# Kernel tuning notes

Measured on AMD Instinct MI355X. Metric: run time of the kernel, lower is better.

Reference implementation:

```python
import jax, jax.numpy as jnp
import numpy as np

DIM = 4096
N_HEADS = 32
N_KV_HEADS = 8
HEAD_DIM = DIM // N_HEADS  # 128
N_REP = N_HEADS // N_KV_HEADS  # 4
HIDDEN = 14336  # 4*dim -> 2/3 -> *1.3 -> round up to multiple of 256
EPS = 1e-6
BSZ, SEQLEN, CACHE_LEN = 1, 2048, 4096
ROPE_THETA = 500000.0


def setup_inputs() -> dict:
    key = jax.random.key(0)
    ks = jax.random.split(key, 16)
    s = 0.02
    x = jax.random.normal(ks[0], (BSZ, SEQLEN, DIM), jnp.float32)
    cache_k = jax.random.normal(ks[1], (BSZ, CACHE_LEN, N_KV_HEADS, HEAD_DIM), jnp.float32)
    cache_v = jax.random.normal(ks[2], (BSZ, CACHE_LEN, N_KV_HEADS, HEAD_DIM), jnp.float32)
    # causal mask over rolling cache: query i may attend to cache slot j <= (CACHE_LEN - SEQLEN) + i
    qi = jnp.arange(SEQLEN)[:, None]
    kj = jnp.arange(CACHE_LEN)[None, :]
    mask = jnp.where(kj <= (CACHE_LEN - SEQLEN) + qi, 0.0, -1e9).astype(jnp.float32)[None, None]
    # rotary freqs (cos/sin pairs) for the new seqlen positions (start of window here)
    inv = 1.0 / (ROPE_THETA ** (jnp.arange(0, HEAD_DIM, 2, dtype=jnp.float32) / HEAD_DIM))
    t = jnp.arange(SEQLEN, dtype=jnp.float32)
    ang = t[:, None] * inv[None, :]  # [S, HEAD_DIM//2]
    freqs_cis = jnp.stack([jnp.cos(ang), jnp.sin(ang)], axis=-1)  # [S, HD//2, 2]
    # params (stored as (in, out))
    wq = jax.random.normal(ks[3], (DIM, N_HEADS * HEAD_DIM), jnp.float32) * s
    wk = jax.random.normal(ks[4], (DIM, N_KV_HEADS * HEAD_DIM), jnp.float32) * s
    wv = jax.random.normal(ks[5], (DIM, N_KV_HEADS * HEAD_DIM), jnp.float32) * s
    wo = jax.random.normal(ks[6], (N_HEADS * HEAD_DIM, DIM), jnp.float32) * s
    w1 = jax.random.normal(ks[7], (DIM, HIDDEN), jnp.float32) * s
    w2 = jax.random.normal(ks[8], (HIDDEN, DIM), jnp.float32) * s
    w3 = jax.random.normal(ks[9], (DIM, HIDDEN), jnp.float32) * s
    attn_norm_w = jnp.ones((DIM,), jnp.float32)
    ffn_norm_w = jnp.ones((DIM,), jnp.float32)
    return dict(x=x, mask=mask, freqs_cis=freqs_cis, cache_k=cache_k, cache_v=cache_v,
                wq=wq, wk=wk, wv=wv, wo=wo, w1=w1, w2=w2, w3=w3,
                attn_norm_w=attn_norm_w, ffn_norm_w=ffn_norm_w)


def rmsnorm(x, w, eps=EPS):
    return x * jax.lax.rsqrt(jnp.mean(x * x, axis=-1, keepdims=True) + eps) * w


def apply_rope(xq, xk, freqs_cis):
    # xq: [B,S,Hq,D], xk: [B,S,Hkv,D]; freqs_cis: [S, D//2, 2]
    cos = freqs_cis[None, :, None, :, 0]  # [1,S,1,D//2]
    sin = freqs_cis[None, :, None, :, 1]
    def rot(t):
        tp = t.reshape(*t.shape[:-1], -1, 2)
        t0, t1 = tp[..., 0], tp[..., 1]
        o0 = t0 * cos - t1 * sin
        o1 = t0 * sin + t1 * cos
        return jnp.stack([o0, o1], axis=-1).reshape(t.shape)
    return rot(xq), rot(xk)


def reference(x, mask, freqs_cis, cache_k, cache_v, wq, wk, wv, wo, w1, w2, w3, attn_norm_w, ffn_norm_w):
    bsz, seqlen, _ = x.shape
    # --- attention norm ---
    xn = rmsnorm(x, attn_norm_w)
    # --- qkv ---
    xq = (xn @ wq).reshape(bsz, seqlen, N_HEADS, HEAD_DIM)
    xk = (xn @ wk).reshape(bsz, seqlen, N_KV_HEADS, HEAD_DIM)
    xv = (xn @ wv).reshape(bsz, seqlen, N_KV_HEADS, HEAD_DIM)
    xq, xk = apply_rope(xq, xk, freqs_cis)
    # --- rolling KV cache ---
    cache_k = jnp.concatenate([cache_k[:, seqlen:], xk], axis=1)  # [B,CL,Hkv,D]
    cache_v = jnp.concatenate([cache_v[:, seqlen:], xv], axis=1)
    keys = jnp.repeat(cache_k[:bsz], N_REP, axis=2)    # [B,CL,Hq,D]
    values = jnp.repeat(cache_v[:bsz], N_REP, axis=2)
    # --- attention ---
    scores = jnp.einsum('bqhd,bkhd->bhqk', xq, keys) / jnp.sqrt(jnp.float32(HEAD_DIM))
    scores = jax.nn.softmax(scores + mask, axis=-1)
    attn = jnp.einsum('bhqk,bkhd->bqhd', scores, values).reshape(bsz, seqlen, -1)
    h = x + attn @ wo
    # --- ffn (SwiGLU) ---
    hn = rmsnorm(h, ffn_norm_w)
    out = h + (jax.nn.silu(hn @ w1) * (hn @ w3)) @ w2
    return (out, cache_k, cache_v)
```

## Files before the change

kernel.cpp:

```cpp
#include <hip/hip_runtime.h>

typedef _Float16 h16;
typedef _Float16 h16x4 __attribute__((ext_vector_type(4)));
typedef _Float16 h16x8 __attribute__((ext_vector_type(8)));
typedef __fp16 fp16x2 __attribute__((ext_vector_type(2)));
typedef float f32x4 __attribute__((ext_vector_type(4)));
typedef float f32x16 __attribute__((ext_vector_type(16)));
typedef unsigned short u16;
typedef unsigned int u32;
typedef unsigned int u32x4 __attribute__((ext_vector_type(4)));

__device__ __forceinline__ f32x4 mfma16(h16x8 a, h16x8 b, f32x4 c) {
  return __builtin_amdgcn_mfma_f32_16x16x32_f16(a, b, c, 0, 0, 0);
}
__device__ __forceinline__ f32x16 mfma32(h16x8 a, h16x8 b, f32x16 c) {
  return __builtin_amdgcn_mfma_f32_32x32x16_f16(a, b, c, 0, 0, 0);
}
__device__ __forceinline__ float fexp2(float x) {
#if __has_builtin(__builtin_amdgcn_exp2f)
  return __builtin_amdgcn_exp2f(x);
#else
  return exp2f(x);
#endif
}
__device__ __forceinline__ u32 pkh(float a, float b) {
  fp16x2 t = __builtin_amdgcn_cvt_pkrtz(a, b);
  return __builtin_bit_cast(u32, t);
}

typedef const __attribute__((address_space(1))) void* gas_p;
typedef __attribute__((address_space(3))) void* las_p;
__device__ __forceinline__ void ldscp16(const void* g, void* l) {
  __builtin_amdgcn_global_load_lds((gas_p)g, (las_p)l, 16, 0, 0);
}
#define VMCNT(n) asm volatile("s_waitcnt vmcnt(" #n ")" ::: "memory")
#define SBAR() asm volatile("s_barrier" ::: "memory")

__global__ __launch_bounds__(256) void rmsnorm_k(
    const float* __restrict__ x, const float* __restrict__ w, h16* __restrict__ out) {
  const int row = blockIdx.x, t = threadIdx.x;
  const float* xr = x + (size_t)row * 4096;
  float4 v[4];
  float ss = 0.f;
#pragma unroll
  for (int j = 0; j < 4; j++) {
    v[j] = *(const float4*)(xr + 4 * t + 1024 * j);
    ss += v[j].x * v[j].x + v[j].y * v[j].y + v[j].z * v[j].z + v[j].w * v[j].w;
  }
#pragma unroll
  for (int off = 1; off < 64; off <<= 1) ss += __shfl_xor(ss, off, 64);
  __shared__ float red[4];
  if ((t & 63) == 0) red[t >> 6] = ss;
  __syncthreads();
  float scale = rsqrtf((red[0] + red[1] + red[2] + red[3]) * (1.f / 4096.f) + 1e-6f);
  h16* orow = out + (size_t)row * 4096;
#pragma unroll
  for (int j = 0; j < 4; j++) {
    float4 wv = *(const float4*)(w + 4 * t + 1024 * j);
    h16x4 o;
    o[0] = (h16)(v[j].x * scale * wv.x);
    o[1] = (h16)(v[j].y * scale * wv.y);
    o[2] = (h16)(v[j].z * scale * wv.z);
    o[3] = (h16)(v[j].w * scale * wv.w);
    *(h16x4*)(orow + 4 * t + 1024 * j) = o;
  }
}

__global__ __launch_bounds__(256) void convw_k(
    const float* __restrict__ W, h16* __restrict__ out, int rowN, int ktiles) {
  __shared__ u16 timg[8192];
  const int t = threadIdx.x, b = blockIdx.x, kt = blockIdx.y;
  const float* src = W + (size_t)(kt * 64) * rowN + b * 128;
#pragma unroll
  for (int i = 0; i < 8; i++) {
    int c = t + (i << 8);
    int krow = c >> 5, nc = (c & 31) << 2;
    float4 v = *(const float4*)(src + (size_t)krow * rowN + nc);
    int kc = krow >> 3, e = krow & 7;
    float vals[4] = {v.x, v.y, v.z, v.w};
#pragma unroll
    for (int j = 0; j < 4; j++) {
      int m = nc + j;
      h16 hv = (h16)vals[j];
      timg[(m << 6) + ((kc ^ (m & 7)) << 3) + e] = __builtin_bit_cast(u16, hv);
    }
  }
  __syncthreads();
  uint4* dst = (uint4*)(out + ((size_t)(b * ktiles + kt) << 13));
  const uint4* s4 = (const uint4*)timg;
#pragma unroll
  for (int i = 0; i < 4; i++) dst[t + (i << 8)] = s4[t + (i << 8)];
}

template <int EPI>
__global__ __launch_bounds__(512, 2) void gemm_k(
    const h16* __restrict__ A, const h16* __restrict__ Wt,
    float* outF, h16* outH, const float* resid, const h16* uin,
    int K, int lda, int ldo, int no0) {
  __shared__ u16 lds[3][24576];
  const int tid = threadIdx.x, lane = tid & 63;
  const int wv = tid >> 6, wr = wv >> 2, wc = wv & 3;
  const int g = lane >> 4, lr = lane & 15;
  const int m0 = blockIdx.y << 7, n0 = blockIdx.x << 8;
  const int ktiles = K >> 6;

  f32x4 acc[4][4];
#pragma unroll
  for (int i = 0; i < 4; i++)
#pragma unroll
    for (int j = 0; j < 4; j++) acc[i][j] = {0.f, 0.f, 0.f, 0.f};

  const int rA = tid >> 3;
  const int kcA = (tid & 7) ^ (rA & 7);
  const h16* gA = A + (size_t)(m0 + rA) * lda + (kcA << 3);
  const h16* gA2 = gA + (size_t)64 * lda;
  const h16* gB0 = Wt + (((size_t)(2 * blockIdx.x) * ktiles) << 13) + tid * 8;
  const h16* gB1 = Wt + (((size_t)(2 * blockIdx.x + 1) * ktiles) << 13) + tid * 8;

  auto issueA = [&](int t) {
    char* base = (char*)lds[t % 3];
    ldscp16(gA + t * 64, base + tid * 16);
    ldscp16(gA2 + t * 64, base + tid * 16 + 8192);
    ldscp16(gB0 + ((size_t)t << 13), base + 16384 + tid * 16);
    ldscp16(gB0 + ((size_t)t << 13) + 4096, base + 16384 + tid * 16 + 8192);
  };
  auto issueB = [&](int t) {
    char* base = (char*)lds[t % 3];
    ldscp16(gB1 + ((size_t)t << 13), base + 32768 + tid * 16);
    ldscp16(gB1 + ((size_t)t << 13) + 4096, base + 32768 + tid * 16 + 8192);
  };

  issueA(0); issueB(0); issueA(1); issueB(1);
  VMCNT(6);
  SBAR();

  for (int t = 0; t < ktiles; ++t) {
    const char* bp = (const char*)lds[t % 3];
    const bool more = (t + 2 < ktiles);
#pragma unroll
    for (int ks = 0; ks < 2; ++ks) {
      h16x8 av[4], bv[4];
      const int cc = (ks << 2) + g;
#pragma unroll
      for (int f = 0; f < 4; f++) {
        int row = (wr << 6) + (f << 4) + lr;
        av[f] = *(const h16x8*)(bp + row * 128 + ((cc ^ (row & 7)) << 4));
        int nr = (wc << 6) + (f << 4) + lr;
        bv[f] = *(const h16x8*)(bp + 16384 + nr * 128 + ((cc ^ (nr & 7)) << 4));
      }
      if (more) {
        if (ks == 0) issueA(t + 2);
        else issueB(t + 2);
      }
      __builtin_amdgcn_s_setprio(1);
#pragma unroll
      for (int fi = 0; fi < 4; fi++)
#pragma unroll
        for (int fj = 0; fj < 4; fj++)
          acc[fi][fj] = mfma16(av[fi], bv[fj], acc[fi][fj]);
      __builtin_amdgcn_s_setprio(0);
    }
    if (t + 1 < ktiles) {
      if (more) VMCNT(6);
      else VMCNT(0);
      SBAR();
    }
  }
#pragma unroll
  for (int fi = 0; fi < 4; fi++) {
    const int row = m0 + (wr << 6) + (fi << 4) + (g << 2);
#pragma unroll
    for (int fj = 0; fj < 4; fj++) {
      const int col = no0 + n0 + (wc << 6) + (fj << 4) + lr;
#pragma unroll
      for (int r = 0; r < 4; r++) {
        float vl = acc[fi][fj][r];
        if constexpr (EPI == 5) {
          if (col < 4096) outH[(size_t)(row + r) * 4096 + col] = (h16)vl;
          else outF[(size_t)(row + r) * 2048 + (col - 4096)] = vl;
        } else {
          size_t idx = (size_t)(row + r) * ldo + col;
          if constexpr (EPI == 1) outH[idx] = (h16)vl;
          else if constexpr (EPI == 2) outF[idx] = resid[idx] + vl;
          else if constexpr (EPI == 3) {
            float u = (float)uin[idx];
            outH[idx] = (h16)((u / (1.f + __expf(-u))) * vl);
          } else outF[idx] = outF[idx] + vl;
        }
      }
    }
  }
}

__global__ __launch_bounds__(256) void rope_q_k(
    const h16* __restrict__ qin, const float* __restrict__ freqs, h16* qout) {
  const int row = blockIdx.x, t = threadIdx.x;
  const float SCL = 0.12751743647239037f;
#pragma unroll
  for (int it = 0; it < 8; ++it) {
    int pid = t + 256 * it;
    int head = pid >> 6, pp = pid & 63;
    size_t idx = (size_t)row * 4096 + head * 128 + 2 * pp;
    float x0 = (float)qin[idx], x1 = (float)qin[idx + 1];
    float cs = freqs[row * 128 + 2 * pp], sn = freqs[row * 128 + 2 * pp + 1];
    qout[idx] = (h16)((x0 * cs - x1 * sn) * SCL);
    qout[idx + 1] = (h16)((x0 * sn + x1 * cs) * SCL);
  }
}

__global__ __launch_bounds__(256) void cache_build_k(
    const float* __restrict__ oldK, const float* __restrict__ oldV,
    const float* __restrict__ kvraw, const float* __restrict__ freqs,
    float* __restrict__ outK, float* __restrict__ outV,
    h16* __restrict__ Kf, h16* __restrict__ Vt) {
  const int rt = blockIdx.x, kvh = blockIdx.y;
  const int r0 = rt * 64, tid = threadIdx.x;
  __shared__ u16 vtile[64][128];
#pragma unroll
  for (int it = 0; it < 16; ++it) {
    int s = tid + 256 * it;
    int rr = s >> 6, pp = s & 63;
    int r = r0 + rr;
    float k0, k1, v0, v1;
    if (r < 2048) {
      const float* kp = oldK + (size_t)(r + 2048) * 1024 + kvh * 128 + 2 * pp;
      k0 = kp[0]; k1 = kp[1];
      const float* vp = oldV + (size_t)(r + 2048) * 1024 + kvh * 128 + 2 * pp;
      v0 = vp[0]; v1 = vp[1];
    } else {
      int tpos = r - 2048;
      const float* kp = kvraw + (size_t)tpos * 2048 + kvh * 128 + 2 * pp;
      float x0 = kp[0], x1 = kp[1];
      float cs = freqs[tpos * 128 + 2 * pp], sn = freqs[tpos * 128 + 2 * pp + 1];
      k0 = x0 * cs - x1 * sn;
      k1 = x0 * sn + x1 * cs;
      const float* vp = kvraw + (size_t)tpos * 2048 + 1024 + kvh * 128 + 2 * pp;
      v0 = vp[0]; v1 = vp[1];
    }
    size_t oidx = (size_t)r * 1024 + kvh * 128 + 2 * pp;
    outK[oidx] = k0; outK[oidx + 1] = k1;
    outV[oidx] = v0; outV[oidx + 1] = v1;
    size_t kfi = (size_t)kvh * 524288 + (size_t)r * 128 + 2 * pp;
    Kf[kfi] = (h16)k0; Kf[kfi + 1] = (h16)k1;
    h16 h0 = (h16)v0, h1 = (h16)v1;
    vtile[rr][2 * pp] = __builtin_bit_cast(u16, h0);
    vtile[rr][2 * pp + 1] = __builtin_bit_cast(u16, h1);
  }
  __syncthreads();
#pragma unroll
  for (int it = 0; it < 4; ++it) {
    int c = tid + 256 * it;
    int d = c >> 3, rg = c & 7;
    u16 tmp[8];
#pragma unroll
    for (int u = 0; u < 8; u++) tmp[u] = vtile[rg * 8 + u][d];
    *(uint4*)((u16*)Vt + (size_t)kvh * 524288 + (size_t)d * 4096 + r0 + rg * 8) =
        *(uint4*)tmp;
  }
}

__global__ __launch_bounds__(256, 2) void attn_k(
    const h16* __restrict__ Q, const h16* __restrict__ Kf,
    const h16* __restrict__ Vt, h16* __restrict__ O) {
  __shared__ u16 skv[2][16384];
  const int qt = 15 - blockIdx.x, h = blockIdx.y;
  const int q0 = qt << 7, kvh = h >> 2;
  const int tid = threadIdx.x, w = tid >> 6, lane = tid & 63;
  const int lq = lane & 31, lh = lane >> 5;
  const h16* Kb = Kf + (size_t)kvh * 524288;
  const h16* Vb = Vt + (size_t)kvh * 524288;
  const int qg = q0 + w * 32 + lq;

  h16x8 qv[8];
  {
    const h16* qp = Q + (size_t)qg * 4096 + h * 128 + (lh << 3);
#pragma unroll
    for (int c = 0; c < 8; c++) qv[c] = *(const h16x8*)(qp + c * 16);
  }
  h16x8 hone;
#pragma unroll
  for (int i = 0; i < 8; i++) hone[i] = (h16)1.0f;
  f32x16 oa[4], ol2;
#pragma unroll
  for (int d = 0; d < 4; d++)
#pragma unroll
    for (int v = 0; v < 16; v++) oa[d][v] = 0.f;
#pragma unroll
  for (int v = 0; v < 16; v++) ol2[v] = 0.f;
  float m2 = -3e38f;
  const int ntiles = 34 + 2 * qt;

  const int jK = tid >> 4, kch = tid & 15;
  const h16* gK = Kb + (size_t)jK * 128 + ((kch ^ (jK & 15)) << 3);
  const int dV = tid >> 3, jch = tid & 7;
  const h16* gV = Vb + (size_t)dV * 4096 + ((jch ^ (dV & 7)) << 3);

  auto issueK = [&](int jt) {
    char* base = (char*)skv[jt & 1];
    const h16* s = gK + (size_t)(jt << 6) * 128;
#pragma unroll
    for (int i = 0; i < 4; i++)
      ldscp16(s + (size_t)i * 2048, base + tid * 16 + i * 4096);
  };
  auto issueV = [&](int jt) {
    char* base = (char*)skv[jt & 1] + 16384;
    const h16* s = gV + (jt << 6);
#pragma unroll
    for (int i = 0; i < 4; i++)
      ldscp16(s + (size_t)i * 131072, base + tid * 16 + i * 4096);
  };

  issueK(0); issueV(0);
  VMCNT(0);
  SBAR();

  for (int jt = 0; jt < ntiles; ++jt) {
    const char* bp = (const char*)skv[jt & 1];
    const bool more = (jt + 1 < ntiles);
    if (more) issueK(jt + 1);
    f32x16 st[2];
#pragma unroll
    for (int jb = 0; jb < 2; jb++) {
      f32x16 s;
#pragma unroll
      for (int v = 0; v < 16; v++) s[v] = 0.f;
      const int jr = jb * 32 + lq;
      __builtin_amdgcn_s_setprio(1);
#pragma unroll
      for (int kc = 0; kc < 8; kc++) {
        h16x8 ak =
            *(const h16x8*)(bp + jr * 256 + ((((kc << 1) + lh) ^ (jr & 15)) << 4));
        s = mfma32(ak, qv[kc], s);
      }
      __builtin_amdgcn_s_setprio(0);
      st[jb] = s;
    }
    if (more) issueV(jt + 1);
    if (jt >= ntiles - 2) {
      const int j0 = jt << 6;
#pragma unroll
      for (int jb = 0; jb < 2; jb++)
#pragma unroll
        for (int v = 0; v < 16; v++) {
          int j = j0 + jb * 32 + (v & 3) + (((v >> 2) & 3) << 3) + (lh << 2);
          if (j > 2048 + qg) st[jb][v] = -1e30f;
        }
    }
    float pm = fmaxf(st[0][0], st[0][1]);
#pragma unroll
    for (int v = 2; v < 16; v += 2) pm = fmaxf(fmaxf(st[0][v], st[0][v + 1]), pm);
#pragma unroll
    for (int v = 0; v < 16; v += 2) pm = fmaxf(fmaxf(st[1][v], st[1][v + 1]), pm);
    pm = fmaxf(pm, __shfl_xor(pm, 32, 64));
    if (__any(pm - m2 > 8.f)) {
      float mn = fmaxf(m2, pm);
      float al = fexp2(m2 - mn);
      m2 = mn;
#pragma unroll
      for (int d = 0; d < 4; d++) oa[d] *= al;
      ol2 *= al;
    }
    u32 pw[2][8];
#pragma unroll
    for (int jb = 0; jb < 2; jb++)
#pragma unroll
      for (int c = 0; c < 4; c++) {
        float p0 = fexp2(st[jb][4 * c] - m2);
        float p1 = fexp2(st[jb][4 * c + 1] - m2);
        float p2 = fexp2(st[jb][4 * c + 2] - m2);
        float p3 = fexp2(st[jb][4 * c + 3] - m2);
        pw[jb][2 * c] = pkh(p0, p1);
        pw[jb][2 * c + 1] = pkh(p2, p3);
      }
    h16x8 pb[4];
#pragma unroll
    for (int kc = 0; kc < 4; kc++) {
      const int jb = kc >> 1, cb = (kc & 1) << 1;
      u32 oa_ = pw[jb][2 * cb], ob_ = pw[jb][2 * cb + 1];
      u32 oc_ = pw[jb][2 * cb + 2], od_ = pw[jb][2 * cb + 3];
      u32 s0 = lh ? oa_ : oc_, s1 = lh ? ob_ : od_;
      u32 r0 = __shfl_xor(s0, 32, 64), r1 = __shfl_xor(s1, 32, 64);
      u32x4 wds = {lh ? r0 : oa_, lh ? r1 : ob_, lh ? oc_ : r0, lh ? od_ : r1};
      pb[kc] = __builtin_bit_cast(h16x8, wds);
    }
    __builtin_amdgcn_s_setprio(1);
#pragma unroll
    for (int d = 0; d < 4; d++) {
      const int dr = (d << 5) + lq;
#pragma unroll
      for (int kc = 0; kc < 4; kc++) {
        h16x8 av = *(const h16x8*)(bp + 16384 + dr * 128 +
                                   ((((kc << 1) + lh) ^ (dr & 7)) << 4));
        oa[d] = mfma32(av, pb[kc], oa[d]);
      }
    }
#pragma unroll
    for (int kc = 0; kc < 4; kc++) ol2 = mfma32(hone, pb[kc], ol2);
    __builtin_amdgcn_s_setprio(0);
    if (more) {
      VMCNT(0);
      SBAR();
    }
  }
  float rl = 1.f / ol2[0];
  h16* Op = O + (size_t)qg * 4096 + h * 128;
#pragma unroll
  for (int d = 0; d < 4; d++)
#pragma unroll
    for (int b = 0; b < 4; b++) {
      h16x4 ov;
#pragma unroll
      for (int i = 0; i < 4; i++) ov[i] = (h16)(oa[d][(b << 2) + i] * rl);
      *(h16x4*)(Op + (d << 5) + (b << 3) + (lh << 2)) = ov;
    }
}

extern "C" void kernel_launch(void* const* d_in, const int* in_sizes, int n_in,
                              void* d_out, int out_size, void* d_ws, size_t ws_size,
                              hipStream_t stream) {
  const float* x = (const float*)d_in[0];
  const float* freqs = (const float*)d_in[2];
  const float* oldK = (const float*)d_in[3];
  const float* oldV = (const float*)d_in[4];
  const float* wq = (const float*)d_in[5];
  const float* wk = (const float*)d_in[6];
  const float* wvp = (const float*)d_in[7];
  const float* wo = (const float*)d_in[8];
  const float* w1 = (const float*)d_in[9];
  const float* w2 = (const float*)d_in[10];
  const float* w3 = (const float*)d_in[11];
  const float* anw = (const float*)d_in[12];
  const float* fnw = (const float*)d_in[13];
  float* out = (float*)d_out;
  float* outK = out + 8388608;
  float* outV = out + 12582912;

  char* ws = (char*)d_ws;
  h16* xn = (h16*)(ws + 0);
  h16* bufW = (h16*)(ws + 16777216);
  float* hbuf = (float*)(ws + 75497472);
  float* kvraw = (float*)(ws + 75497472);
  h16* kf = (h16*)(ws + 92274688);
  h16* vt = (h16*)(ws + 100663296);
  h16* ub = (h16*)(ws + 109051904);
  h16* qraw = (h16*)(ws + 109051904);
  h16* attnb = (h16*)(ws + 125829120);

  rmsnorm_k<<<2048, 256, 0, stream>>>(x, anw, xn);
  convw_k<<<dim3(32, 64), 256, 0, stream>>>(wq, bufW, 4096, 64);
  convw_k<<<dim3(8, 64), 256, 0, stream>>>(wk, bufW + ((size_t)32 * 64 << 13), 1024, 64);
  convw_k<<<dim3(8, 64), 256, 0, stream>>>(wvp, bufW + ((size_t)40 * 64 << 13), 1024, 64);
  gemm_k<5><<<dim3(24, 16), 512, 0, stream>>>(xn, bufW, kvraw, qraw, nullptr,
                                              nullptr, 4096, 4096, 0, 0);
  rope_q_k<<<2048, 256, 0, stream>>>(qraw, freqs, qraw);
  cache_build_k<<<dim3(64, 8), 256, 0, stream>>>(oldK, oldV, kvraw, freqs, outK,
                                                 outV, kf, vt);
  attn_k<<<dim3(16, 32), 256, 0, stream>>>(qraw, kf, vt, attnb);
  convw_k<<<dim3(32, 64), 256, 0, stream>>>(wo, bufW, 4096, 64);
  gemm_k<2><<<dim3(16, 16), 512, 0, stream>>>(attnb, bufW, hbuf, nullptr, x,
                                              nullptr, 4096, 4096, 4096, 0);
  rmsnorm_k<<<2048, 256, 0, stream>>>(hbuf, fnw, xn);
  convw_k<<<dim3(56, 64), 256, 0, stream>>>(w1, bufW, 14336, 64);
  gemm_k<1><<<dim3(28, 16), 512, 0, stream>>>(xn, bufW, nullptr, ub, nullptr,
                                              nullptr, 4096, 4096, 14336, 0);
  convw_k<<<dim3(56, 64), 256, 0, stream>>>(w1 + 7168, bufW, 14336, 64);
  gemm_k<1><<<dim3(28, 16), 512, 0, stream>>>(xn, bufW, nullptr, ub, nullptr,
                                              nullptr, 4096, 4096, 14336, 7168);
  convw_k<<<dim3(56, 64), 256, 0, stream>>>(w3, bufW, 14336, 64);
  gemm_k<3><<<dim3(28, 16), 512, 0, stream>>>(xn, bufW, nullptr, ub, nullptr, ub,
                                              4096, 4096, 14336, 0);
  convw_k<<<dim3(56, 64), 256, 0, stream>>>(w3 + 7168, bufW, 14336, 64);
  gemm_k<3><<<dim3(28, 16), 512, 0, stream>>>(xn, bufW, nullptr, ub, nullptr, ub,
                                              4096, 4096, 14336, 7168);
  convw_k<<<dim3(32, 112), 256, 0, stream>>>(w2, bufW, 4096, 112);
  gemm_k<2><<<dim3(16, 16), 512, 0, stream>>>(ub, bufW, out, nullptr, hbuf,
                                              nullptr, 7168, 14336, 4096, 0);
  convw_k<<<dim3(32, 112), 256, 0, stream>>>(w2 + (size_t)7168 * 4096, bufW, 4096, 112);
  gemm_k<4><<<dim3(16, 16), 512, 0, stream>>>(ub + 7168, bufW, out, nullptr,
                                              nullptr, nullptr, 7168, 14336, 4096, 0);
}
```

Baseline: 1.533 ms.

## Enlarge GEMM block tile to 256x256 with quadrant-staged double-buffered pipeline

The GEMM kernel changes from a 128x256 block tile with a 3-stage LDS ring to a 256x256 tile with a 2-stage double buffer. Each K-step is split into four quadrant MFMA phases, and loads for the next tile's A and B quadrants are interleaved between phases. The goal is to double operand reuse per block and cut global/L2 traffic per FLOP. In exchange each wave holds twice the accumulators (128 regs), which puts register pressure on the 2-blocks-per-CU bound. The grid is also halved, which may hurt wave balance across CUs for the smaller GEMMs.

Measured after the change: 1.718 ms. +12.1%, slower.

```diff
diff --git a/kernel.cpp b/kernel.cpp
--- a/kernel.cpp
+++ b/kernel.cpp
@@ -93,103 +93,159 @@
 }
 
 template <int EPI>
-__global__ __launch_bounds__(512, 2) void gemm_k(
+__global__ __launch_bounds__(512, 2) void gemm8_k(
     const h16* __restrict__ A, const h16* __restrict__ Wt,
     float* outF, h16* outH, const float* resid, const h16* uin,
     int K, int lda, int ldo, int no0) {
-  __shared__ u16 lds[3][24576];
+  __shared__ u16 lds[2][32768];
   const int tid = threadIdx.x, lane = tid & 63;
-  const int wv = tid >> 6, wr = wv >> 2, wc = wv & 3;
+  const int wv = tid >> 6, wm = wv >> 2, wn = wv & 3;
   const int g = lane >> 4, lr = lane & 15;
-  const int m0 = blockIdx.y << 7, n0 = blockIdx.x << 8;
-  const int ktiles = K >> 6;
-
-  f32x4 acc[4][4];
-#pragma unroll
-  for (int i = 0; i < 4; i++)
-#pragma unroll
-    for (int j = 0; j < 4; j++) acc[i][j] = {0.f, 0.f, 0.f, 0.f};
-
-  const int rA = tid >> 3;
-  const int kcA = (tid & 7) ^ (rA & 7);
-  const h16* gA = A + (size_t)(m0 + rA) * lda + (kcA << 3);
-  const h16* gA2 = gA + (size_t)64 * lda;
-  const h16* gB0 = Wt + (((size_t)(2 * blockIdx.x) * ktiles) << 13) + tid * 8;
-  const h16* gB1 = Wt + (((size_t)(2 * blockIdx.x + 1) * ktiles) << 13) + tid * 8;
-
-  auto issueA = [&](int t) {
-    char* base = (char*)lds[t % 3];
-    ldscp16(gA + t * 64, base + tid * 16);
-    ldscp16(gA2 + t * 64, base + tid * 16 + 8192);
-    ldscp16(gB0 + ((size_t)t << 13), base + 16384 + tid * 16);
-    ldscp16(gB0 + ((size_t)t << 13) + 4096, base + 16384 + tid * 16 + 8192);
+  const int m0 = blockIdx.y << 8, n0 = blockIdx.x << 8;
+  const int nkt = K >> 6;
+
+  f32x4 acc[2][2][4][2];
+#pragma unroll
+  for (int a = 0; a < 2; a++)
+#pragma unroll
+    for (int b = 0; b < 2; b++)
+#pragma unroll
+      for (int f = 0; f < 4; f++)
+#pragma unroll
+        for (int e = 0; e < 2; e++) acc[a][b][f][e] = {0.f, 0.f, 0.f, 0.f};
+
+  const int rr = tid >> 3, ch0 = tid & 7;
+  auto stageA = [&](int t, int qm) {
+    char* dst = (char*)lds[t & 1] + qm * 16384 + tid * 16;
+#pragma unroll
+    for (int i = 0; i < 2; i++) {
+      int r = i * 64 + rr;
+      const h16* src =
+          A + (size_t)(m0 + qm * 128 + r) * lda + t * 64 + ((ch0 ^ (r & 7)) << 3);
+      ldscp16(src, dst + i * 8192);
+    }
   };
-  auto issueB = [&](int t) {
-    char* base = (char*)lds[t % 3];
-    ldscp16(gB1 + ((size_t)t << 13), base + 32768 + tid * 16);
-    ldscp16(gB1 + ((size_t)t << 13) + 4096, base + 32768 + tid * 16 + 8192);
+  auto stageB = [&](int t, int qn) {
+    char* dst = (char*)lds[t & 1] + 32768 + qn * 16384 + tid * 16;
+    const h16* src =
+        Wt + (((size_t)(2 * blockIdx.x + qn) * nkt + t) << 13) + tid * 8;
+    ldscp16(src, dst);
+    ldscp16(src + 4096, dst + 8192);
   };
 
-  issueA(0); issueB(0); issueA(1); issueB(1);
-  VMCNT(6);
-  SBAR();
-
-  for (int t = 0; t < ktiles; ++t) {
-    const char* bp = (const char*)lds[t % 3];
-    const bool more = (t + 2 < ktiles);
-#pragma unroll
-    for (int ks = 0; ks < 2; ++ks) {
-      h16x8 av[4], bv[4];
-      const int cc = (ks << 2) + g;
+  stageA(0, 0); stageB(0, 0); stageB(0, 1); stageA(0, 1);
+
+  for (int t = 0; t < nkt; ++t) {
+    const char* bp = (const char*)lds[t & 1];
+    const bool more = (t + 1 < nkt);
+    h16x8 av[2][4], bv0[2][2], bv1[2][2];
+    VMCNT(4);
+    SBAR();
+    if (more) stageA(t + 1, 0);
+#pragma unroll
+    for (int ks = 0; ks < 2; ks++) {
+      const int cc = ks * 4 + g;
 #pragma unroll
       for (int f = 0; f < 4; f++) {
-        int row = (wr << 6) + (f << 4) + lr;
-        av[f] = *(const h16x8*)(bp + row * 128 + ((cc ^ (row & 7)) << 4));
-        int nr = (wc << 6) + (f << 4) + lr;
-        bv[f] = *(const h16x8*)(bp + 16384 + nr * 128 + ((cc ^ (nr & 7)) << 4));
-      }
-      if (more) {
-        if (ks == 0) issueA(t + 2);
-        else issueB(t + 2);
-      }
-      __builtin_amdgcn_s_setprio(1);
-#pragma unroll
-      for (int fi = 0; fi < 4; fi++)
-#pragma unroll
-        for (int fj = 0; fj < 4; fj++)
-          acc[fi][fj] = mfma16(av[fi], bv[fj], acc[fi][fj]);
-      __builtin_amdgcn_s_setprio(0);
-    }
-    if (t + 1 < ktiles) {
-      if (more) VMCNT(6);
-      else VMCNT(0);
-      SBAR();
-    }
-  }
-#pragma unroll
-  for (int fi = 0; fi < 4; fi++) {
-    const int row = m0 + (wr << 6) + (fi << 4) + (g << 2);
-#pragma unroll
-    for (int fj = 0; fj < 4; fj++) {
-      const int col = no0 + n0 + (wc << 6) + (fj << 4) + lr;
-#pragma unroll
-      for (int r = 0; r < 4; r++) {
-        float vl = acc[fi][fj][r];
-        if constexpr (EPI == 5) {
-          if (col < 4096) outH[(size_t)(row + r) * 4096 + col] = (h16)vl;
-          else outF[(size_t)(row + r) * 2048 + (col - 4096)] = vl;
-        } else {
-          size_t idx = (size_t)(row + r) * ldo + col;
-          if constexpr (EPI == 1) outH[idx] = (h16)vl;
-          else if constexpr (EPI == 2) outF[idx] = resid[idx] + vl;
-          else if constexpr (EPI == 3) {
-            float u = (float)uin[idx];
-            outH[idx] = (h16)((u / (1.f + __expf(-u))) * vl);
-          } else outF[idx] = outF[idx] + vl;
+        int r = wm * 64 + f * 16 + lr;
+        av[ks][f] = *(const h16x8*)(bp + r * 128 + ((cc ^ (r & 7)) << 4));
+      }
+#pragma unroll
+      for (int e = 0; e < 2; e++) {
+        int c = wn * 32 + e * 16 + lr;
+        bv0[ks][e] = *(const h16x8*)(bp + 32768 + c * 128 + ((cc ^ (c & 7)) << 4));
+      }
+    }
+    __builtin_amdgcn_s_setprio(1);
+#pragma unroll
+    for (int ks = 0; ks < 2; ks++)
+#pragma unroll
+      for (int f = 0; f < 4; f++)
+#pragma unroll
+        for (int e = 0; e < 2; e++)
+          acc[0][0][f][e] = mfma16(av[ks][f], bv0[ks][e], acc[0][0][f][e]);
+    __builtin_amdgcn_s_setprio(0);
+    if (more) { VMCNT(4); } else { VMCNT(2); }
+    SBAR();
+    if (more) stageB(t + 1, 0);
+#pragma unroll
+    for (int ks = 0; ks < 2; ks++) {
+      const int cc = ks * 4 + g;
+#pragma unroll
+      for (int e = 0; e < 2; e++) {
+        int c = 128 + wn * 32 + e * 16 + lr;
+        bv1[ks][e] = *(const h16x8*)(bp + 32768 + c * 128 + ((cc ^ (c & 7)) << 4));
+      }
+    }
+    __builtin_amdgcn_s_setprio(1);
+#pragma unroll
+    for (int ks = 0; ks < 2; ks++)
+#pragma unroll
+      for (int f = 0; f < 4; f++)
+#pragma unroll
+        for (int e = 0; e < 2; e++)
+          acc[0][1][f][e] = mfma16(av[ks][f], bv1[ks][e], acc[0][1][f][e]);
+    __builtin_amdgcn_s_setprio(0);
+    if (more) { VMCNT(4); } else { VMCNT(0); }
+    SBAR();
+    if (more) stageB(t + 1, 1);
+#pragma unroll
+    for (int ks = 0; ks < 2; ks++) {
+      const int cc = ks * 4 + g;
+#pragma unroll
+      for (int f = 0; f < 4; f++) {
+        int r = 128 + wm * 64 + f * 16 + lr;
+        av[ks][f] = *(const h16x8*)(bp + r * 128 + ((cc ^ (r & 7)) << 4));
+      }
+    }
+    __builtin_amdgcn_s_setprio(1);
+#pragma unroll
+    for (int ks = 0; ks < 2; ks++)
+#pragma unroll
+      for (int f = 0; f < 4; f++)
+#pragma unroll
+        for (int e = 0; e < 2; e++)
+          acc[1][0][f][e] = mfma16(av[ks][f], bv0[ks][e], acc[1][0][f][e]);
+    __builtin_amdgcn_s_setprio(0);
+    if (more) stageA(t + 1, 1);
+    __builtin_amdgcn_s_setprio(1);
+#pragma unroll
+    for (int ks = 0; ks < 2; ks++)
+#pragma unroll
+      for (int f = 0; f < 4; f++)
+#pragma unroll
+        for (int e = 0; e < 2; e++)
+          acc[1][1][f][e] = mfma16(av[ks][f], bv1[ks][e], acc[1][1][f][e]);
+    __builtin_amdgcn_s_setprio(0);
+  }
+#pragma unroll
+  for (int qm = 0; qm < 2; qm++)
+#pragma unroll
+    for (int qn = 0; qn < 2; qn++)
+#pragma unroll
+      for (int f = 0; f < 4; f++) {
+        const int row = m0 + qm * 128 + wm * 64 + f * 16 + (g << 2);
+#pragma unroll
+        for (int e = 0; e < 2; e++) {
+          const int col = no0 + n0 + qn * 128 + wn * 32 + e * 16 + lr;
+#pragma unroll
+          for (int r = 0; r < 4; r++) {
+            float vl = acc[qm][qn][f][e][r];
+            if constexpr (EPI == 5) {
+              if (col < 4096) outH[(size_t)(row + r) * 4096 + col] = (h16)vl;
+              else outF[(size_t)(row + r) * 2048 + (col - 4096)] = vl;
+            } else {
+              size_t idx = (size_t)(row + r) * ldo + col;
+              if constexpr (EPI == 1) outH[idx] = (h16)vl;
+              else if constexpr (EPI == 2) outF[idx] = resid[idx] + vl;
+              else if constexpr (EPI == 3) {
+                float u = (float)uin[idx];
+                outH[idx] = (h16)((u / (1.f + __expf(-u))) * vl);
+              } else outF[idx] = outF[idx] + vl;
+            }
+          }
         }
       }
-    }
-  }
 }
 
 __global__ __launch_bounds__(256) void rope_q_k(
@@ -450,32 +506,32 @@
   convw_k<<<dim3(32, 64), 256, 0, stream>>>(wq, bufW, 4096, 64);
   convw_k<<<dim3(8, 64), 256, 0, stream>>>(wk, bufW + ((size_t)32 * 64 << 13), 1024, 64);
   convw_k<<<dim3(8, 64), 256, 0, stream>>>(wvp, bufW + ((size_t)40 * 64 << 13), 1024, 64);
-  gemm_k<5><<<dim3(24, 16), 512, 0, stream>>>(xn, bufW, kvraw, qraw, nullptr,
+  gemm8_k<5><<<dim3(24, 8), 512, 0, stream>>>(xn, bufW, kvraw, qraw, nullptr,
                                               nullptr, 4096, 4096, 0, 0);
   rope_q_k<<<2048, 256, 0, stream>>>(qraw, freqs, qraw);
   cache_build_k<<<dim3(64, 8), 256, 0, stream>>>(oldK, oldV, kvraw, freqs, outK,
                                                  outV, kf, vt);
   attn_k<<<dim3(16, 32), 256, 0, stream>>>(qraw, kf, vt, attnb);
   convw_k<<<dim3(32, 64), 256, 0, stream>>>(wo, bufW, 4096, 64);
-  gemm_k<2><<<dim3(16, 16), 512, 0, stream>>>(attnb, bufW, hbuf, nullptr, x,
+  gemm8_k<2><<<dim3(16, 8), 512, 0, stream>>>(attnb, bufW, hbuf, nullptr, x,
                                               nullptr, 4096, 4096, 4096, 0);
   rmsnorm_k<<<2048, 256, 0, stream>>>(hbuf, fnw, xn);
   convw_k<<<dim3(56, 64), 256, 0, stream>>>(w1, bufW, 14336, 64);
-  gemm_k<1><<<dim3(28, 16), 512, 0, stream>>>(xn, bufW, nullptr, ub, nullptr,
+  gemm8_k<1><<<dim3(28, 8), 512, 0, stream>>>(xn, bufW, nullptr, ub, nullptr,
                                               nullptr, 4096, 4096, 14336, 0);
   convw_k<<<dim3(56, 64), 256, 0, stream>>>(w1 + 7168, bufW, 14336, 64);
-  gemm_k<1><<<dim3(28, 16), 512, 0, stream>>>(xn, bufW, nullptr, ub, nullptr,
+  gemm8_k<1><<<dim3(28, 8), 512, 0, stream>>>(xn, bufW, nullptr, ub, nullptr,
                                               nullptr, 4096, 4096, 14336, 7168);
   convw_k<<<dim3(56, 64), 256, 0, stream>>>(w3, bufW, 14336, 64);
-  gemm_k<3><<<dim3(28, 16), 512, 0, stream>>>(xn, bufW, nullptr, ub, nullptr, ub,
+  gemm8_k<3><<<dim3(28, 8), 512, 0, stream>>>(xn, bufW, nullptr, ub, nullptr, ub,
                                               4096, 4096, 14336, 0);
   convw_k<<<dim3(56, 64), 256, 0, stream>>>(w3 + 7168, bufW, 14336, 64);
-  gemm_k<3><<<dim3(28, 16), 512, 0, stream>>>(xn, bufW, nullptr, ub, nullptr, ub,
+  gemm8_k<3><<<dim3(28, 8), 512, 0, stream>>>(xn, bufW, nullptr, ub, nullptr, ub,
                                               4096, 4096, 14336, 7168);
   convw_k<<<dim3(32, 112), 256, 0, stream>>>(w2, bufW, 4096, 112);
-  gemm_k<2><<<dim3(16, 16), 512, 0, stream>>>(ub, bufW, out, nullptr, hbuf,
+  gemm8_k<2><<<dim3(16, 8), 512, 0, stream>>>(ub, bufW, out, nullptr, hbuf,
                                               nullptr, 7168, 14336, 4096, 0);
   convw_k<<<dim3(32, 112), 256, 0, stream>>>(w2 + (size_t)7168 * 4096, bufW, 4096, 112);
-  gemm_k<4><<<dim3(16, 16), 512, 0, stream>>>(ub + 7168, bufW, out, nullptr,
+  gemm8_k<4><<<dim3(16, 8), 512, 0, stream>>>(ub + 7168, bufW, out, nullptr,
                                               nullptr, nullptr, 7168, 14336, 4096, 0);
 }
```

## Switch GEMM tiles to 256x128 with a 4x2 wave grid and barriered pipeline

Applied to the files above, without the earlier changes.

The GEMM now uses 256(M)x128(N) block tiles instead of 128x256, with waves laid out 4x2 over M and N. A-tile loads become four 16-byte copies per thread and B loads two. The main loop is restructured so each k-substep reads LDS fragments, hits a barrier, then runs MFMAs, with the next tile's A and B prefetches issued at separate points. Launch bounds drop to one block per SM-equivalent, and the grids are adjusted. This changes the block grid counts and the balance between global traffic and MFMA issue, at the cost of extra barriers per k-tile and lower occupancy.

New measurement: 1.562 ms. No clear change (+1.9%).

```diff
diff --git a/kernel.cpp b/kernel.cpp
--- a/kernel.cpp
+++ b/kernel.cpp
@@ -93,16 +93,16 @@
 }
 
 template <int EPI>
-__global__ __launch_bounds__(512, 2) void gemm_k(
+__global__ __launch_bounds__(512, 1) void gemm12_k(
     const h16* __restrict__ A, const h16* __restrict__ Wt,
     float* outF, h16* outH, const float* resid, const h16* uin,
     int K, int lda, int ldo, int no0) {
   __shared__ u16 lds[3][24576];
   const int tid = threadIdx.x, lane = tid & 63;
-  const int wv = tid >> 6, wr = wv >> 2, wc = wv & 3;
+  const int wv = tid >> 6, wm = wv >> 1, wn = wv & 1;
   const int g = lane >> 4, lr = lane & 15;
-  const int m0 = blockIdx.y << 7, n0 = blockIdx.x << 8;
-  const int ktiles = K >> 6;
+  const int m0 = blockIdx.y << 8, n0 = blockIdx.x << 7;
+  const int nkt = K >> 6;
 
   f32x4 acc[4][4];
 #pragma unroll
@@ -110,68 +110,76 @@
 #pragma unroll
     for (int j = 0; j < 4; j++) acc[i][j] = {0.f, 0.f, 0.f, 0.f};
 
-  const int rA = tid >> 3;
-  const int kcA = (tid & 7) ^ (rA & 7);
-  const h16* gA = A + (size_t)(m0 + rA) * lda + (kcA << 3);
-  const h16* gA2 = gA + (size_t)64 * lda;
-  const h16* gB0 = Wt + (((size_t)(2 * blockIdx.x) * ktiles) << 13) + tid * 8;
-  const h16* gB1 = Wt + (((size_t)(2 * blockIdx.x + 1) * ktiles) << 13) + tid * 8;
-
+  const int rr8 = tid >> 3, ch8 = tid & 7;
   auto issueA = [&](int t) {
-    char* base = (char*)lds[t % 3];
-    ldscp16(gA + t * 64, base + tid * 16);
-    ldscp16(gA2 + t * 64, base + tid * 16 + 8192);
-    ldscp16(gB0 + ((size_t)t << 13), base + 16384 + tid * 16);
-    ldscp16(gB0 + ((size_t)t << 13) + 4096, base + 16384 + tid * 16 + 8192);
+    char* dst = (char*)lds[t % 3] + tid * 16;
+#pragma unroll
+    for (int i = 0; i < 4; i++) {
+      int r = i * 64 + rr8;
+      const h16* src = A + (size_t)(m0 + r) * lda + t * 64 + ((ch8 ^ (r & 7)) << 3);
+      ldscp16(src, dst + i * 8192);
+    }
   };
   auto issueB = [&](int t) {
-    char* base = (char*)lds[t % 3];
-    ldscp16(gB1 + ((size_t)t << 13), base + 32768 + tid * 16);
-    ldscp16(gB1 + ((size_t)t << 13) + 4096, base + 32768 + tid * 16 + 8192);
+    char* dst = (char*)lds[t % 3] + 32768 + tid * 16;
+    const h16* src = Wt + (((size_t)blockIdx.x * nkt + t) << 13) + tid * 8;
+    ldscp16(src, dst);
+    ldscp16(src + 4096, dst + 8192);
   };
 
   issueA(0); issueB(0); issueA(1); issueB(1);
-  VMCNT(6);
-  SBAR();
-
-  for (int t = 0; t < ktiles; ++t) {
+
+  for (int t = 0; t < nkt; ++t) {
     const char* bp = (const char*)lds[t % 3];
-    const bool more = (t + 2 < ktiles);
-#pragma unroll
-    for (int ks = 0; ks < 2; ++ks) {
-      h16x8 av[4], bv[4];
-      const int cc = (ks << 2) + g;
+    const bool m1 = t + 1 < nkt, m2 = t + 2 < nkt;
+    if (m1) { VMCNT(6); } else { VMCNT(0); }
+    SBAR();
+    h16x8 av[4], bv[4];
+    if (m2) issueA(t + 2);
+    {
+      const int cc = g;
 #pragma unroll
       for (int f = 0; f < 4; f++) {
-        int row = (wr << 6) + (f << 4) + lr;
-        av[f] = *(const h16x8*)(bp + row * 128 + ((cc ^ (row & 7)) << 4));
-        int nr = (wc << 6) + (f << 4) + lr;
-        bv[f] = *(const h16x8*)(bp + 16384 + nr * 128 + ((cc ^ (nr & 7)) << 4));
-      }
-      if (more) {
-        if (ks == 0) issueA(t + 2);
-        else issueB(t + 2);
-      }
-      __builtin_amdgcn_s_setprio(1);
-#pragma unroll
-      for (int fi = 0; fi < 4; fi++)
-#pragma unroll
-        for (int fj = 0; fj < 4; fj++)
-          acc[fi][fj] = mfma16(av[fi], bv[fj], acc[fi][fj]);
-      __builtin_amdgcn_s_setprio(0);
-    }
-    if (t + 1 < ktiles) {
-      if (more) VMCNT(6);
-      else VMCNT(0);
-      SBAR();
-    }
+        int r = wm * 64 + f * 16 + lr;
+        av[f] = *(const h16x8*)(bp + r * 128 + ((cc ^ (r & 7)) << 4));
+        int c = wn * 64 + f * 16 + lr;
+        bv[f] = *(const h16x8*)(bp + 32768 + c * 128 + ((cc ^ (c & 7)) << 4));
+      }
+    }
+    SBAR();
+    __builtin_amdgcn_s_setprio(1);
+#pragma unroll
+    for (int fi = 0; fi < 4; fi++)
+#pragma unroll
+      for (int fj = 0; fj < 4; fj++)
+        acc[fi][fj] = mfma16(av[fi], bv[fj], acc[fi][fj]);
+    __builtin_amdgcn_s_setprio(0);
+    if (m2) issueB(t + 2);
+    {
+      const int cc = 4 + g;
+#pragma unroll
+      for (int f = 0; f < 4; f++) {
+        int r = wm * 64 + f * 16 + lr;
+        av[f] = *(const h16x8*)(bp + r * 128 + ((cc ^ (r & 7)) << 4));
+        int c = wn * 64 + f * 16 + lr;
+        bv[f] = *(const h16x8*)(bp + 32768 + c * 128 + ((cc ^ (c & 7)) << 4));
+      }
+    }
+    SBAR();
+    __builtin_amdgcn_s_setprio(1);
+#pragma unroll
+    for (int fi = 0; fi < 4; fi++)
+#pragma unroll
+      for (int fj = 0; fj < 4; fj++)
+        acc[fi][fj] = mfma16(av[fi], bv[fj], acc[fi][fj]);
+    __builtin_amdgcn_s_setprio(0);
   }
 #pragma unroll
   for (int fi = 0; fi < 4; fi++) {
-    const int row = m0 + (wr << 6) + (fi << 4) + (g << 2);
+    const int row = m0 + wm * 64 + fi * 16 + (g << 2);
 #pragma unroll
     for (int fj = 0; fj < 4; fj++) {
-      const int col = no0 + n0 + (wc << 6) + (fj << 4) + lr;
+      const int col = no0 + n0 + wn * 64 + fj * 16 + lr;
 #pragma unroll
       for (int r = 0; r < 4; r++) {
         float vl = acc[fi][fj][r];
@@ -450,32 +458,32 @@
   convw_k<<<dim3(32, 64), 256, 0, stream>>>(wq, bufW, 4096, 64);
   convw_k<<<dim3(8, 64), 256, 0, stream>>>(wk, bufW + ((size_t)32 * 64 << 13), 1024, 64);
   convw_k<<<dim3(8, 64), 256, 0, stream>>>(wvp, bufW + ((size_t)40 * 64 << 13), 1024, 64);
-  gemm_k<5><<<dim3(24, 16), 512, 0, stream>>>(xn, bufW, kvraw, qraw, nullptr,
-                                              nullptr, 4096, 4096, 0, 0);
+  gemm12_k<5><<<dim3(48, 8), 512, 0, stream>>>(xn, bufW, kvraw, qraw, nullptr,
+                                               nullptr, 4096, 4096, 0, 0);
   rope_q_k<<<2048, 256, 0, stream>>>(qraw, freqs, qraw);
   cache_build_k<<<dim3(64, 8), 256, 0, stream>>>(oldK, oldV, kvraw, freqs, outK,
                                                  outV, kf, vt);
   attn_k<<<dim3(16, 32), 256, 0, stream>>>(qraw, kf, vt, attnb);
   convw_k<<<dim3(32, 64), 256, 0, stream>>>(wo, bufW, 4096, 64);
-  gemm_k<2><<<dim3(16, 16), 512, 0, stream>>>(attnb, bufW, hbuf, nullptr, x,
-                                              nullptr, 4096, 4096, 4096, 0);
+  gemm12_k<2><<<dim3(32, 8), 512, 0, stream>>>(attnb, bufW, hbuf, nullptr, x,
+                                               nullptr, 4096, 4096, 4096, 0);
   rmsnorm_k<<<2048, 256, 0, stream>>>(hbuf, fnw, xn);
   convw_k<<<dim3(56, 64), 256, 0, stream>>>(w1, bufW, 14336, 64);
-  gemm_k<1><<<dim3(28, 16), 512, 0, stream>>>(xn, bufW, nullptr, ub, nullptr,
-                                              nullptr, 4096, 4096, 14336, 0);
+  gemm12_k<1><<<dim3(56, 8), 512, 0, stream>>>(xn, bufW, nullptr, ub, nullptr,
+                                               nullptr, 4096, 4096, 14336, 0);
   convw_k<<<dim3(56, 64), 256, 0, stream>>>(w1 + 7168, bufW, 14336, 64);
-  gemm_k<1><<<dim3(28, 16), 512, 0, stream>>>(xn, bufW, nullptr, ub, nullptr,
-                                              nullptr, 4096, 4096, 14336, 7168);
+  gemm12_k<1><<<dim3(56, 8), 512, 0, stream>>>(xn, bufW, nullptr, ub, nullptr,
+                                               nullptr, 4096, 4096, 14336, 7168);
   convw_k<<<dim3(56, 64), 256, 0, stream>>>(w3, bufW, 14336, 64);
-  gemm_k<3><<<dim3(28, 16), 512, 0, stream>>>(xn, bufW, nullptr, ub, nullptr, ub,
-                                              4096, 4096, 14336, 0);
+  gemm12_k<3><<<dim3(56, 8), 512, 0, stream>>>(xn, bufW, nullptr, ub, nullptr, ub,
+                                               4096, 4096, 14336, 0);
   convw_k<<<dim3(56, 64), 256, 0, stream>>>(w3 + 7168, bufW, 14336, 64);
-  gemm_k<3><<<dim3(28, 16), 512, 0, stream>>>(xn, bufW, nullptr, ub, nullptr, ub,
-                                              4096, 4096, 14336, 7168);
+  gemm12_k<3><<<dim3(56, 8), 512, 0, stream>>>(xn, bufW, nullptr, ub, nullptr, ub,
+                                               4096, 4096, 14336, 7168);
   convw_k<<<dim3(32, 112), 256, 0, stream>>>(w2, bufW, 4096, 112);
-  gemm_k<2><<<dim3(16, 16), 512, 0, stream>>>(ub, bufW, out, nullptr, hbuf,
-                                              nullptr, 7168, 14336, 4096, 0);
+  gemm12_k<2><<<dim3(32, 8), 512, 0, stream>>>(ub, bufW, out, nullptr, hbuf,
+                                               nullptr, 7168, 14336, 4096, 0);
   convw_k<<<dim3(32, 112), 256, 0, stream>>>(w2 + (size_t)7168 * 4096, bufW, 4096, 112);
-  gemm_k<4><<<dim3(16, 16), 512, 0, stream>>>(ub + 7168, bufW, out, nullptr,
-                                              nullptr, nullptr, 7168, 14336, 4096, 0);
-}
+  gemm12_k<4><<<dim3(32, 8), 512, 0, stream>>>(ub + 7168, bufW, out, nullptr,
+                                               nullptr, nullptr, 7168, 14336, 4096, 0);
+}
```
